# Kernel tuning notes

Measured on AMD Instinct MI355X. Metric: run time of the kernel, lower is better.

## Reference

```python
import jax, jax.numpy as jnp
import numpy as np

B_GRAPHS = 256
N_PER = 512
N = B_GRAPHS * N_PER            # 131072 nodes
E = 1048576                     # edges (avg degree 8)
H = 64                          # hidden_dim
L = 3                           # num_layers
R = 128                         # rnn_dim
NODE_IN = 2
EDGE_IN = 2
OUT = 2
JK = L * H


def setup_inputs() -> dict:
    key = jax.random.key(0)
    ks = jax.random.split(key, 40)
    # intra-graph random edges
    g = jax.random.randint(ks[0], (E,), 0, B_GRAPHS)
    src = g * N_PER + jax.random.randint(ks[1], (E,), 0, N_PER)
    dst = g * N_PER + jax.random.randint(ks[2], (E,), 0, N_PER)
    edge_index = jnp.stack([src, dst]).astype(jnp.int64)
    batch = jnp.repeat(jnp.arange(B_GRAPHS, dtype=jnp.int64), N_PER)

    p = lambda k, shp: jax.random.normal(k, shp, jnp.float32) * 0.1
    return dict(
        x=jax.random.normal(ks[3], (N, NODE_IN), jnp.float32),
        edge_attr=jax.random.normal(ks[4], (E, EDGE_IN), jnp.float32),
        node_W=p(ks[5], (NODE_IN, H)), node_b=p(ks[6], (H,)),
        edgeemb_W=p(ks[7], (EDGE_IN, H)), edgeemb_b=p(ks[8], (H,)),
        gat_W=p(ks[9], (L, H, H)), gat_Wedge=p(ks[10], (L, H, H)),
        gat_att_src=p(ks[11], (L, H)), gat_att_dst=p(ks[12], (L, H)),
        gat_att_edge=p(ks[13], (L, H)), gat_b=p(ks[14], (L, H)),
        gru_wih_f=p(ks[15], (3 * R, JK)), gru_whh_f=p(ks[16], (3 * R, R)),
        gru_bih_f=p(ks[17], (3 * R,)), gru_bhh_f=p(ks[18], (3 * R,)),
        gru_wih_b=p(ks[19], (3 * R, JK)), gru_whh_b=p(ks[20], (3 * R, R)),
        gru_bih_b=p(ks[21], (3 * R,)), gru_bhh_b=p(ks[22], (3 * R,)),
        head_W1=p(ks[23], (2 * R, 64)), head_b1=p(ks[24], (64,)),
        head_W2=p(ks[25], (64, OUT)), head_b2=p(ks[26], (OUT,)),
        edge_index=edge_index, batch=batch,
    )


def _gru_dir(xs, wih, whh, bih, bhh):
    # xs: [T, B, F] -> outputs [T, B, R]  (PyTorch GRU cell equations)
    gx = xs @ wih.T + bih  # precompute input gates [T, B, 3R]
    h0 = jnp.zeros((xs.shape[1], R), xs.dtype)

    def step(h, g):
        gh = h @ whh.T + bhh
        r = jax.nn.sigmoid(g[..., :R] + gh[..., :R])
        z = jax.nn.sigmoid(g[..., R:2 * R] + gh[..., R:2 * R])
        n = jnp.tanh(g[..., 2 * R:] + r * gh[..., 2 * R:])
        hn = (1.0 - z) * n + z * h
        return hn, hn

    _, ys = jax.lax.scan(step, h0, gx)
    return ys


def _forward(x, edge_attr, node_W, node_b, edgeemb_W, edgeemb_b,
             gat_W, gat_Wedge, gat_att_src, gat_att_dst, gat_att_edge, gat_b,
             gru_wih_f, gru_whh_f, gru_bih_f, gru_bhh_f,
             gru_wih_b, gru_whh_b, gru_bih_b, gru_bhh_b,
             head_W1, head_b1, head_W2, head_b2, edge_index, batch):
    src, dst = edge_index[0], edge_index[1]
    h = x @ node_W + node_b                     # [N, H]
    e = edge_attr @ edgeemb_W + edgeemb_b       # [E, H]

    # PyG GATConv default add_self_loops=True, fill_value='mean':
    # self-loop edge feature = mean of incoming edge features per node
    ones = jnp.ones((E,), e.dtype)
    deg = jax.ops.segment_sum(ones, dst, num_segments=N)
    e_loop = jax.ops.segment_sum(e, dst, num_segments=N) / jnp.maximum(deg, 1.0)[:, None]
    ar = jnp.arange(N, dtype=src.dtype)
    srcF = jnp.concatenate([src, ar])
    dstF = jnp.concatenate([dst, ar])
    eF = jnp.concatenate([e, e_loop], axis=0)   # [E+N, H]

    outs = []
    for l in range(L):
        xp = h @ gat_W[l]                                   # [N, H]
        a_s = xp @ gat_att_src[l]                           # [N]
        a_d = xp @ gat_att_dst[l]                           # [N]
        a_e = (eF @ gat_Wedge[l]) @ gat_att_edge[l]         # [E+N]
        alpha = jax.nn.leaky_relu(a_s[srcF] + a_d[dstF] + a_e, 0.2)
        m = jax.ops.segment_max(alpha, dstF, num_segments=N)
        ex = jnp.exp(alpha - m[dstF])
        den = jax.ops.segment_sum(ex, dstF, num_segments=N)
        w = ex / den[dstF]                                  # segment softmax
        agg = jax.ops.segment_sum(w[:, None] * xp[srcF], dstF, num_segments=N) + gat_b[l]
        h = jax.nn.leaky_relu(agg, 0.01)                    # F.leaky_relu default slope
        outs.append(h)

    h_jk = jnp.concatenate(outs, axis=-1)                   # [N, JK]
    # to_dense_batch: sorted equal-size graphs -> dense reshape, mask all True
    dense = h_jk.reshape(B_GRAPHS, N_PER, JK)
    xs = dense.transpose(1, 0, 2)                           # [T, B, JK]
    yf = _gru_dir(xs, gru_wih_f, gru_whh_f, gru_bih_f, gru_bhh_f)
    yb = _gru_dir(xs[::-1], gru_wih_b, gru_whh_b, gru_bih_b, gru_bhh_b)[::-1]
    rnn_out = jnp.concatenate([yf, yb], axis=-1).transpose(1, 0, 2)  # [B, T, 2R]
    out = jax.nn.relu(rnn_out @ head_W1 + head_b1) @ head_W2 + head_b2
    return out.reshape(N, OUT)                              # out[mask], mask full


def reference(x, edge_attr, node_W, node_b, edgeemb_W, edgeemb_b,
              gat_W, gat_Wedge, gat_att_src, gat_att_dst, gat_att_edge, gat_b,
              gru_wih_f, gru_whh_f, gru_bih_f, gru_bhh_f,
              gru_wih_b, gru_whh_b, gru_bih_b, gru_bhh_b,
              head_W1, head_b1, head_W2, head_b2, edge_index, batch):
    return _forward(x, edge_attr, node_W, node_b, edgeemb_W, edgeemb_b,
                    gat_W, gat_Wedge, gat_att_src, gat_att_dst, gat_att_edge, gat_b,
                    gru_wih_f, gru_whh_f, gru_bih_f, gru_bhh_f,
                    gru_wih_b, gru_whh_b, gru_bih_b, gru_bhh_b,
                    head_W1, head_b1, head_W2, head_b2, edge_index, batch)
```

## Files before the change

### kernel.cpp

```cpp
#include <hip/hip_runtime.h>
#include <cstdint>
#include <cstddef>

typedef _Float16 half_t;
typedef _Float16 half8 __attribute__((ext_vector_type(8)));
typedef float f32x4 __attribute__((ext_vector_type(4)));

constexpr int NN = 131072;
constexpr int NE = 1048576;
constexpr int NPER = 512;

#define DEVINL __device__ __forceinline__

DEVINL float sigm_(float x){ float e = __expf(-x); return __builtin_amdgcn_rcpf(1.f+e); }
DEVINL float tanh_(float x){
  x = fminf(15.f, fmaxf(-15.f, x));
  float e = __expf(-2.f*x);
  return (1.f-e)*__builtin_amdgcn_rcpf(1.f+e);
}

#define LDS_BARRIER() asm volatile("s_waitcnt lgkmcnt(0)\ns_barrier" ::: "memory")


__global__ void const_kernel(const float* __restrict__ gatWe,
                             const float* __restrict__ attE, const float* __restrict__ eW,
                             const float* __restrict__ eb, float* __restrict__ cc){
  int l = blockIdx.x, k = threadIdx.x;
  const float* Wel = gatWe + l*4096;
  float s3=0.f;
  for (int j=0;j<64;j++) s3 += Wel[k*64+j]*attE[l*64+j];
  float c0 = eW[k]*s3, c1 = eW[64+k]*s3, cb = eb[k]*s3;
  for (int off=1; off<64; off<<=1){
    c0 += __shfl_xor(c0,off); c1 += __shfl_xor(c1,off); cb += __shfl_xor(cb,off);
  }
  if (k==0){ cc[l]=c0; cc[3+l]=c1; cc[6+l]=cb; }
}

__global__ void prep_pack(const float* __restrict__ wih_f, const float* __restrict__ wih_b,
                          const float* __restrict__ head_W1, const float* __restrict__ gat_W,
                          const float* __restrict__ bih_f, const float* __restrict__ bih_b,
                          const float* __restrict__ whh_f, const float* __restrict__ whh_b,
                          half_t* __restrict__ BcombT, half_t* __restrict__ W1T,
                          half_t* __restrict__ BTgat, float* __restrict__ bias_comb,
                          half_t* __restrict__ whh16){
  int gid = blockIdx.x*256 + threadIdx.x;
  if (gid < 147456){
    int j = gid/192, k = gid%192;
    float v = (j<384)? wih_f[j*192+k] : wih_b[(j-384)*192+k];
    BcombT[gid] = (half_t)v;
  } else if (gid < 163840){
    int i = gid - 147456;
    int n = i>>8, k = i&255;
    W1T[i] = (half_t)head_W1[k*64+n];
  } else if (gid < 176128){
    int i = gid - 163840;
    int l = i>>12, r = i&4095;
    int n = r>>6, k = r&63;
    BTgat[i] = (half_t)gat_W[l*4096 + k*64 + n];
  } else if (gid < 176896){
    int i = gid - 176128;
    int j = (i<384)? i : i-384;
    bias_comb[i] = (i<384)? bih_f[j] : bih_b[j];
  } else if (gid < 275200){
    int i = gid - 176896;
    float v = (i<49152)? whh_f[i] : whh_b[i-49152];
    whh16[i] = (half_t)v;
  }
}

__global__ void bias_fold(const float* __restrict__ bhh_f, const float* __restrict__ bhh_b,
                          float* __restrict__ bias_comb){
  int i = threadIdx.x + blockIdx.x*256;
  if (i < 256)      bias_comb[i]       += bhh_f[i];
  else if (i < 512) bias_comb[i+128]   += bhh_b[i-256];
}

__global__ __launch_bounds__(256) void embed_kernel(const float* __restrict__ x,
                            const float* __restrict__ nW, const float* __restrict__ nb,
                            half_t* __restrict__ h){
  int gid = blockIdx.x*256 + threadIdx.x;
  int n = gid>>6, j = gid&63;
  float v = x[2*n]*nW[j] + x[2*n+1]*nW[64+j] + nb[j];
  h[(size_t)n*64+j] = (half_t)v;
}

__global__ __launch_bounds__(256) void deg_count(const int* __restrict__ ei,
                          int* __restrict__ deg, int* __restrict__ tmp){
  int e = blockIdx.x*256 + threadIdx.x;
  int dt = ei[NE+e];
  tmp[e] = atomicAdd(&deg[dt],1);
}

__global__ __launch_bounds__(256) void scan1(const int* __restrict__ deg, int* __restrict__ rowstart,
                      int* __restrict__ bsum){
  __shared__ int sc[256];
  int b=blockIdx.x, t=threadIdx.x, i=b*256+t;
  int v=deg[i]; sc[t]=v; __syncthreads();
  for (int off=1; off<256; off<<=1){
    int tv = (t>=off)? sc[t-off] : 0;
    __syncthreads(); sc[t]+=tv; __syncthreads();
  }
  rowstart[i]=sc[t]-v;
  if (t==255) bsum[b]=sc[255];
}
__global__ void scan2(int* __restrict__ bsum){
  __shared__ int sc[512];
  int t=threadIdx.x; int v=bsum[t]; sc[t]=v; __syncthreads();
  for (int off=1; off<512; off<<=1){
    int tv = (t>=off)? sc[t-off] : 0;
    __syncthreads(); sc[t]+=tv; __syncthreads();
  }
  bsum[t]=sc[t]-v;
}
__global__ __launch_bounds__(256) void scan3(int* __restrict__ rowstart, const int* __restrict__ bsum){
  int b=blockIdx.x, t=threadIdx.x, i=b*256+t;
  rowstart[i]+=bsum[b];
}

__global__ __launch_bounds__(256) void fill2(const int* __restrict__ ei, const float* __restrict__ ea,
                      const int* __restrict__ rowstart, const int* __restrict__ tmp,
                      int4* __restrict__ rec){
  int e = blockIdx.x*256 + threadIdx.x;
  int dt = ei[NE+e];
  int slot = rowstart[dt] + tmp[e];
  int4 r;
  r.x = ei[e];
  r.y = __float_as_int(ea[2*e]);
  r.z = __float_as_int(ea[2*e+1]);
  r.w = dt;
  rec[slot] = r;
}

__global__ __launch_bounds__(256) void means_kernel(const int* __restrict__ deg, const int* __restrict__ rowstart,
                         const int4* __restrict__ rec, float2* __restrict__ m01){
  int n = blockIdx.x*256 + threadIdx.x;
  int st = rowstart[n], cnt = deg[n];
  float s0=0.f, s1=0.f;
  for (int i=0;i<cnt;i++){
    int4 r = rec[st+i];
    s0 += __int_as_float(r.y);
    s1 += __int_as_float(r.z);
  }
  float inv = 1.f/(float)max(cnt,1);
  float2 m; m.x = s0*inv; m.y = s1*inv;
  m01[n] = m;
}

__global__ __launch_bounds__(256) void gemm_xp(const half_t* __restrict__ A, int lda,
                        const half_t* __restrict__ BT,
                        const float* __restrict__ attS, const float* __restrict__ attD,
                        half_t* __restrict__ xp, float* __restrict__ a_s, float* __restrict__ a_d){
  __shared__ half_t As[128*32];
  __shared__ half_t Bs[64*32];
  const int tid = threadIdx.x, m0 = blockIdx.x*128;
  const int w = tid>>6, lane = tid&63;
  const int lm = lane&15, quad = lane>>4;
  const int wm0 = w*32;
  f32x4 acc[2][4] = {};
  for (int k0=0;k0<64;k0+=32){
    {
      const int c0 = tid*2;
      #pragma unroll
      for (int u=0;u<2;u++){
        int c=c0+u; int row=c>>2; int off=(c&3)*8;
        *(half8*)(&As[row*32+off]) = *(const half8*)(&A[(size_t)(m0+row)*lda + k0 + off]);
      }
      int c=tid; int row=c>>2; int off=(c&3)*8;
      *(half8*)(&Bs[row*32+off]) = *(const half8*)(&BT[(size_t)row*64 + k0 + off]);
    }
    __syncthreads();
    half8 af[2], bf[4];
    #pragma unroll
    for (int nt=0;nt<4;nt++) bf[nt] = *(const half8*)(&Bs[(nt*16+lm)*32 + quad*8]);
    #pragma unroll
    for (int mt=0;mt<2;mt++) af[mt] = *(const half8*)(&As[(wm0+mt*16+lm)*32 + quad*8]);
    #pragma unroll
    for (int mt=0;mt<2;mt++)
      #pragma unroll
      for (int nt=0;nt<4;nt++)
        acc[mt][nt] = __builtin_amdgcn_mfma_f32_16x16x32_f16(af[mt], bf[nt], acc[mt][nt], 0,0,0);
    __syncthreads();
  }
  float vsv[4], vdv[4];
  #pragma unroll
  for (int nt=0;nt<4;nt++){ vsv[nt]=attS[nt*16+lm]; vdv[nt]=attD[nt*16+lm]; }
  #pragma unroll
  for (int mt=0;mt<2;mt++)
   #pragma unroll
   for (int r=0;r<4;r++){
    int m = m0+wm0+mt*16+quad*4+r;
    float ps=0.f, pd=0.f;
    #pragma unroll
    for (int nt=0;nt<4;nt++){
      float v = acc[mt][nt][r];
      xp[(size_t)m*64 + nt*16+lm] = (half_t)v;
      ps += v*vsv[nt]; pd += v*vdv[nt];
    }
    ps += __shfl_xor(ps,1); ps += __shfl_xor(ps,2); ps += __shfl_xor(ps,4); ps += __shfl_xor(ps,8);
    pd += __shfl_xor(pd,1); pd += __shfl_xor(pd,2); pd += __shfl_xor(pd,4); pd += __shfl_xor(pd,8);
    if (lm==0){ a_s[m]=ps; a_d[m]=pd; }
  }
}

__global__ __launch_bounds__(256) void edge_w(const int4* __restrict__ rec,
                       const float* __restrict__ a_s, const float* __restrict__ a_d,
                       const float* __restrict__ cc, int l, int2* __restrict__ sw,
                       const int* __restrict__ deg, const float2* __restrict__ m01,
                       float* __restrict__ wsf){
  int b = blockIdx.x;
  if (b < 4096){
    int s = b*256 + threadIdx.x;
    int4 r = rec[s];
    float al = a_s[r.x] + a_d[r.w]
             + __int_as_float(r.y)*cc[l] + __int_as_float(r.z)*cc[3+l] + cc[6+l];
    al = al>0.f? al : 0.2f*al;
    int2 o;
    o.x = (r.x & 511) | ((r.w & 127) << 16);
    o.y = __float_as_int(__expf(al));
    sw[s] = o;
  } else {
    int n = (b-4096)*256 + threadIdx.x;
    int cnt = deg[n];
    float2 m = m01[n];
    float ael = cnt? (m.x*cc[l] + m.y*cc[3+l] + cc[6+l]) : 0.f;
    float asl = a_s[n] + a_d[n] + ael;
    asl = asl>0.f? asl : 0.2f*asl;
    wsf[n] = __expf(asl);
  }
}

constexpr int SWCAP = 1536;
__global__ __launch_bounds__(512,4) void agg_lds(const int* __restrict__ rowstart, const int* __restrict__ deg,
                          const int2* __restrict__ sw, const float* __restrict__ wsf, int l,
                          const half_t* __restrict__ xp, const float* __restrict__ bias,
                          half_t* __restrict__ hjk){
  __shared__ int2  swl[SWCAP];
  __shared__ float nwsf[128];
  __shared__ int   ncnt[128];
  const int tid = threadIdx.x;
  const int nbase = blockIdx.x*128;
  const half_t* __restrict__ xpg = xp + ((size_t)(nbase >> 9))*32768;
  const int segst = rowstart[nbase];
  const int segend = rowstart[nbase+127] + deg[nbase+127];
  const int segcnt = segend - segst;
  const int w = tid>>6, lane = tid&63;
  int scap = segcnt < SWCAP ? segcnt : SWCAP;
  for (int i=tid; i<scap; i+=512) swl[i] = sw[segst+i];
  if (tid < 128){
    nwsf[tid] = wsf[nbase + tid];
    ncnt[tid] = deg[nbase + tid];
  }
  const int e0 = rowstart[nbase + w*16] - segst;
  const int e1 = (w==7) ? segcnt : (rowstart[nbase + w*16 + 16] - segst);
  __syncthreads();
  const float bv = bias[lane];
  const int nlb = nbase & 511;

  auto flush = [&](int cur, float acc, float den){
    float wv = nwsf[cur];
    float xs = (float)xpg[(size_t)(nlb + cur)*64 + lane];
    float v = (acc + wv*xs)/(den + wv) + bv;
    v = v>0.f? v : 0.01f*v;
    hjk[(size_t)(nbase + cur)*192 + l*64 + lane] = (half_t)v;
  };

  if (segcnt <= SWCAP){
    if (e0 < e1){
      int2 p = swl[e0];
      float xv = (float)xpg[(size_t)(p.x & 511)*64 + lane];
      int cur = p.x >> 16;
      float acc = 0.f, den = 0.f;
      for (int e = e0; e < e1; ++e){
        int en = (e+1 < e1) ? e+1 : e;
        int2 pn = swl[en];
        float xvn = (float)xpg[(size_t)(pn.x & 511)*64 + lane];
        int dl = p.x >> 16;
        if (dl != cur){
          flush(cur, acc, den);
          cur = dl; acc = 0.f; den = 0.f;
        }
        float ww = __int_as_float(p.y);
        acc += ww*xv; den += ww;
        p = pn; xv = xvn;
      }
      flush(cur, acc, den);
    }
    #pragma unroll
    for (int i=0;i<16;i++){
      int li = w*16+i;
      if (ncnt[li]==0) flush(li, 0.f, 0.f);
    }
  } else {
    if (e0 < e1){
      int2 p = sw[segst+e0];
      float xv = (float)xpg[(size_t)(p.x & 511)*64 + lane];
      int cur = p.x >> 16;
      float acc = 0.f, den = 0.f;
      for (int e = e0; e < e1; ++e){
        int en = (e+1 < e1) ? e+1 : e;
        int2 pn = sw[segst+en];
        float xvn = (float)xpg[(size_t)(pn.x & 511)*64 + lane];
        int dl = p.x >> 16;
        if (dl != cur){
          flush(cur, acc, den);
          cur = dl; acc = 0.f; den = 0.f;
        }
        float ww = __int_as_float(p.y);
        acc += ww*xv; den += ww;
        p = pn; xv = xvn;
      }
      flush(cur, acc, den);
    }
    #pragma unroll
    for (int i=0;i<16;i++){
      int li = w*16+i;
      if (ncnt[li]==0) flush(li, 0.f, 0.f);
    }
  }
}

__global__ __launch_bounds__(256) void gemm_head(const half_t* __restrict__ A,
                        const half_t* __restrict__ W1T, const float* __restrict__ b1,
                        const float* __restrict__ W2, const float* __restrict__ b2,
                        float* __restrict__ out){
  __shared__ half_t As[128*32];
  __shared__ half_t Bs[64*32];
  const int tid = threadIdx.x, m0 = blockIdx.x*128;
  const int w = tid>>6, lane = tid&63;
  const int lm = lane&15, quad = lane>>4;
  const int wm0 = w*32;
  f32x4 acc[2][4] = {};
  for (int k0=0;k0<256;k0+=32){
    {
      const int c0 = tid*2;
      #pragma unroll
      for (int u=0;u<2;u++){
        int c=c0+u; int row=c>>2; int off=(c&3)*8;
        *(half8*)(&As[row*32+off]) = *(const half8*)(&A[(size_t)(m0+row)*256 + k0 + off]);
      }
      int c=tid; int row=c>>2; int off=(c&3)*8;
      *(half8*)(&Bs[row*32+off]) = *(const half8*)(&W1T[(size_t)row*256 + k0 + off]);
    }
    __syncthreads();
    half8 af[2], bf[4];
    #pragma unroll
    for (int nt=0;nt<4;nt++) bf[nt] = *(const half8*)(&Bs[(nt*16+lm)*32 + quad*8]);
    #pragma unroll
    for (int mt=0;mt<2;mt++) af[mt] = *(const half8*)(&As[(wm0+mt*16+lm)*32 + quad*8]);
    #pragma unroll
    for (int mt=0;mt<2;mt++)
      #pragma unroll
      for (int nt=0;nt<4;nt++)
        acc[mt][nt] = __builtin_amdgcn_mfma_f32_16x16x32_f16(af[mt], bf[nt], acc[mt][nt], 0,0,0);
    __syncthreads();
  }
  float b1v[4], w20[4], w21[4];
  #pragma unroll
  for (int nt=0;nt<4;nt++){
    int n = nt*16+lm;
    b1v[nt]=b1[n]; w20[nt]=W2[n*2]; w21[nt]=W2[n*2+1];
  }
  float b20=b2[0], b21=b2[1];
  #pragma unroll
  for (int mt=0;mt<2;mt++)
   #pragma unroll
   for (int r=0;r<4;r++){
    int m = m0+wm0+mt*16+quad*4+r;
    float p0=0.f, p1=0.f;
    #pragma unroll
    for (int nt=0;nt<4;nt++){
      float v = acc[mt][nt][r] + b1v[nt];
      v = v>0.f? v : 0.f;
      p0 += v*w20[nt]; p1 += v*w21[nt];
    }
    p0 += __shfl_xor(p0,1); p0 += __shfl_xor(p0,2); p0 += __shfl_xor(p0,4); p0 += __shfl_xor(p0,8);
    p1 += __shfl_xor(p1,1); p1 += __shfl_xor(p1,2); p1 += __shfl_xor(p1,4); p1 += __shfl_xor(p1,8);
    if (lm==0){
      out[(size_t)m*2]   = p0 + b20;
      out[(size_t)m*2+1] = p1 + b21;
    }
  }
}

__global__ __launch_bounds__(512,1) void gru_fused(
    const half_t* __restrict__ whh16, const float* __restrict__ bhh_f, const float* __restrict__ bhh_b,
    const half_t* __restrict__ gxf, const half_t* __restrict__ gxb,
    float* __restrict__ hstate, half_t* __restrict__ y, int c, int gruBlocks,
    const half_t* __restrict__ hjk, const half_t* __restrict__ BcombT, const float* __restrict__ biasc,
    half_t* __restrict__ gxf_n, half_t* __restrict__ gxb_n, int s0f, int s0b){
  __shared__ __align__(16) char SMEM[16384];
  const int bid = blockIdx.x;
  const int tid = threadIdx.x;
  if (bid < gruBlocks){
    __builtin_amdgcn_s_setprio(1);
    auto& H = *(half_t (*)[2][16][132])SMEM;
    half_t* slab0 = (half_t*)(SMEM + 8448);
    half_t* slab1 = (half_t*)(SMEM + 8448 + 3072);

    const int d = bid >> 6, gblk = bid & 63;
    const half_t* __restrict__ gx = d ? gxb : gxf;
    const float* bhh = d ? bhh_b : bhh_f;
    const int w = tid >> 6, lane = tid & 63;
    const int l15 = lane & 15, quad = lane >> 4;
    const int unit = w*16 + l15;

    half8 bf[3][4];
    float bhn = bhh[256 + unit];
    {
      const half_t* wbase = whh16 + (size_t)d*49152;
      #pragma unroll
      for (int g=0; g<3; g++){
        const half_t* wp = wbase + (size_t)(g*128 + unit)*128;
        #pragma unroll
        for (int kk=0; kk<4; kk++)
          bf[g][kk] = *(const half8*)(wp + kk*32 + quad*8);
      }
    }

    float hreg = hstate[((size_t)d*256 + gblk*4 + quad)*128 + unit];

    const bool loader = (w >= 4 && w < 7);
    const int jsl = d ? -384 : 384;
    int idx8 = 0;
    const half_t* srcp = nullptr;
    if (loader){
      int idx = (w-4)*64 + lane;
      int g_loc = idx/48, o = idx - g_loc*48;
      idx8 = idx*8;
      int j0 = d ? 127 : 0;
      srcp = gx + ((size_t)(gblk*4 + g_loc)*128 + j0)*384 + o*8;
    }

    const int cgg = tid >> 6;
    const int cpart = (tid & 63)*2;
    const int pos0 = d ? (511 - c*128) : (c*128);
    const int ystep = d ? -256 : 256;
    half_t* yptr = y + ((size_t)(gblk*4 + cgg)*512 + pos0)*256 + d*128 + cpart;

    for (int i=tid; i<2112; i+=512) ((uint*)SMEM)[i] = 0;
    LDS_BARRIER();
    H[0][quad*4][unit] = (half_t)hreg;
    half8 lvA, lvB;
    if (loader){
      lvA = *(const half8*)srcp; srcp += jsl;
      *(half8*)(slab0 + idx8) = lvA;
      lvB = *(const half8*)srcp; srcp += jsl;
    }
    LDS_BARRIER();

    auto stepf = [&](const half_t* cs, half_t* ns, int rd, int wr2,
                     half8& lvI, half8& lvW, bool pfi, bool pfw, bool cp){
      if (loader && pfi){ lvI = *(const half8*)srcp; srcp += jsl; }
      if (cp && tid < 256){
        uint hv = *(const uint*)&H[rd][cgg*4][cpart];
        *(uint*)yptr = hv;
        yptr += ystep;
      }
      float g0 = (float)cs[quad*384 + unit];
      float g1 = (float)cs[quad*384 + 128 + unit];
      float g2 = (float)cs[quad*384 + 256 + unit];
      half8 af[4] = {};
      if ((l15 & 3) == 0){
        #pragma unroll
        for (int kk=0; kk<4; kk++)
          af[kk] = *(const half8*)&H[rd][l15][kk*32 + quad*8];
      }
      f32x4 P[3] = {};
      #pragma unroll
      for (int kk=0; kk<4; kk++)
        #pragma unroll
        for (int g=0; g<3; g++)
          P[g] = __builtin_amdgcn_mfma_f32_16x16x32_f16(af[kk], bf[g][kk], P[g], 0,0,0);
      float rr = sigm_(g0 + P[0][0]);
      float zz = sigm_(g1 + P[1][0]);
      float nn = tanh_(g2 + rr*(P[2][0] + bhn));
      float hn = nn + zz*(hreg - nn);
      hreg = hn;
      H[wr2][quad*4][unit] = (half_t)hn;
      if (loader && pfw) *(half8*)(ns + idx8) = lvW;
      LDS_BARRIER();
    };

    stepf(slab0, slab1, 0,1, lvA, lvB, true,  true,  false);
    stepf(slab1, slab0, 1,0, lvB, lvA, true,  true,  true);
    for (int it=1; it<63; it++){
      stepf(slab0, slab1, 0,1, lvA, lvB, true, true, true);
      stepf(slab1, slab0, 1,0, lvB, lvA, true, true, true);
    }
    stepf(slab0, slab1, 0,1, lvA, lvB, false, true,  true);
    stepf(slab1, slab0, 1,0, lvB, lvA, false, false, true);
    if (tid < 256){
      uint hv = *(const uint*)&H[0][cgg*4][cpart];
      *(uint*)yptr = hv;
    }
    __builtin_amdgcn_s_setprio(0);
    hstate[((size_t)d*256 + gblk*4 + quad)*128 + unit] = hreg;
  } else {
    half_t* As = (half_t*)SMEM;
    half_t* Bs = (half_t*)(SMEM + 8192);
    const int gb = bid - gruBlocks;
    const int bx = gb & 255, by = gb >> 8;
    const int m0 = bx*128;
    const bool back = by >= 3;
    const int n0 = (back ? by-3 : by)*128;
    const int step0 = back ? s0b : s0f;
    half_t* C = back ? gxb_n : gxf_n;
    const half_t* BTh = BcombT + (back ? (size_t)384*192 : 0);
    const float* bh = biasc + (back ? 384 : 0);
    const int w = tid>>6, lane = tid&63;
    const int lm = lane&15, quad = lane>>4;
    const int wm0 = (w>>2)*64, wn0 = (w&3)*32;
    f32x4 acc[4][2] = {};
    for (int k0=0; k0<192; k0+=32){
      {
        int cidx = tid; int row = cidx>>2; int off = (cidx&3)*8;
        int m = m0+row;
        size_t arow = (size_t)(m>>7)*512 + step0 + (m&127);
        *(half8*)(&As[row*32+off]) = *(const half8*)(&hjk[arow*192 + k0 + off]);
        *(half8*)(&Bs[row*32+off]) = *(const half8*)(&BTh[(size_t)(n0+row)*192 + k0 + off]);
      }
      __syncthreads();
      half8 af[4], bfr[2];
      #pragma unroll
      for (int nt=0;nt<2;nt++) bfr[nt] = *(const half8*)(&Bs[(wn0+nt*16+lm)*32 + quad*8]);
      #pragma unroll
      for (int mt=0;mt<4;mt++) af[mt] = *(const half8*)(&As[(wm0+mt*16+lm)*32 + quad*8]);
      #pragma unroll
      for (int mt=0;mt<4;mt++)
        #pragma unroll
        for (int nt=0;nt<2;nt++)
          acc[mt][nt] = __builtin_amdgcn_mfma_f32_16x16x32_f16(af[mt], bfr[nt], acc[mt][nt], 0,0,0);
      __syncthreads();
    }
    #pragma unroll
    for (int mt=0;mt<4;mt++)
     #pragma unroll
     for (int nt=0;nt<2;nt++)
      #pragma unroll
      for (int r=0;r<4;r++){
        int m = m0+wm0+mt*16+quad*4+r;
        int n = n0+wn0+nt*16+lm;
        float v = acc[mt][nt][r] + bh[n];
        C[(size_t)m*384 + n] = (half_t)v;
      }
  }
}

extern "C" void kernel_launch(void* const* d_in, const int* in_sizes, int n_in,
                              void* d_out, int out_size, void* d_ws, size_t ws_size,
                              hipStream_t stream) {
  const float* x       = (const float*)d_in[0];
  const float* ea      = (const float*)d_in[1];
  const float* node_W  = (const float*)d_in[2];
  const float* node_b  = (const float*)d_in[3];
  const float* eW      = (const float*)d_in[4];
  const float* eb      = (const float*)d_in[5];
  const float* gat_W   = (const float*)d_in[6];
  const float* gat_We  = (const float*)d_in[7];
  const float* attS    = (const float*)d_in[8];
  const float* attD    = (const float*)d_in[9];
  const float* attE    = (const float*)d_in[10];
  const float* gat_b   = (const float*)d_in[11];
  const float* wih_f   = (const float*)d_in[12];
  const float* whh_f   = (const float*)d_in[13];
  const float* bih_f   = (const float*)d_in[14];
  const float* bhh_f   = (const float*)d_in[15];
  const float* wih_b   = (const float*)d_in[16];
  const float* whh_b   = (const float*)d_in[17];
  const float* bih_b   = (const float*)d_in[18];
  const float* bhh_b   = (const float*)d_in[19];
  const float* head_W1 = (const float*)d_in[20];
  const float* head_b1 = (const float*)d_in[21];
  const float* head_W2 = (const float*)d_in[22];
  const float* head_b2 = (const float*)d_in[23];
  const int*   ei      = (const int*)d_in[24];
  float* out = (float*)d_out;
  char* ws = (char*)d_ws;
  (void)in_sizes; (void)n_in; (void)out_size; (void)ws_size;

  size_t o = 0;
  auto alloc = [&](size_t bytes)->size_t{ size_t r=o; o += (bytes+255)&~(size_t)255; return r; };
  size_t o_cc     = alloc(16*4);
  size_t o_biasc  = alloc(768*4);
  size_t o_BcombT = alloc((size_t)768*192*2);
  size_t o_BTgat  = alloc((size_t)3*4096*2);
  size_t o_W1T    = alloc((size_t)64*256*2);
  size_t o_whh16  = alloc((size_t)2*49152*2);
  size_t o_hstate = alloc((size_t)2*256*128*4);
  size_t shared_base = o;

  size_t o_deg    = alloc((size_t)NN*4);
  size_t zero_end = o;
  size_t o_tmp    = alloc((size_t)NE*4);
  size_t o_rows   = alloc((size_t)NN*4);
  size_t o_bsum   = alloc(512*4);
  size_t o_rec    = alloc((size_t)NE*16);
  size_t o_sw     = alloc((size_t)NE*8);
  size_t o_m01    = alloc((size_t)NN*8);
  size_t o_as     = alloc((size_t)NN*4);
  size_t o_ad     = alloc((size_t)NN*4);
  size_t o_wsf    = alloc((size_t)NN*4);
  size_t o_h      = alloc((size_t)NN*64*2);
  size_t o_xp     = alloc((size_t)NN*64*2);
  size_t gat_end  = o;
  size_t gat_size = gat_end - shared_base;

  const size_t GXC    = (size_t)256*128*384*2;
  const size_t HJK_SZ = (size_t)NN*192*2;
  size_t shared_sz = gat_size > 4*GXC ? gat_size : 4*GXC;
  size_t o_gx0f = shared_base;
  size_t o_gx0b = shared_base + GXC;
  size_t o_gx1f = shared_base + 2*GXC;
  size_t o_gx1b = shared_base + 3*GXC;
  size_t o_hjk = shared_base + shared_sz;
  size_t o_y   = o_hjk + HJK_SZ;

  int*    deg    = (int*)(ws+o_deg);
  int*    tmp    = (int*)(ws+o_tmp);
  int*    rows   = (int*)(ws+o_rows);
  int*    bsum   = (int*)(ws+o_bsum);
  int4*   rec    = (int4*)(ws+o_rec);
  int2*   sw     = (int2*)(ws+o_sw);
  float2* m01    = (float2*)(ws+o_m01);
  float*  a_s    = (float*)(ws+o_as);
  float*  a_d    = (float*)(ws+o_ad);
  float*  wsf    = (float*)(ws+o_wsf);
  float*  cc     = (float*)(ws+o_cc);
  float*  biasc  = (float*)(ws+o_biasc);
  half_t* h      = (half_t*)(ws+o_h);
  half_t* xp     = (half_t*)(ws+o_xp);
  half_t* hjk    = (half_t*)(ws+o_hjk);
  half_t* BcombT = (half_t*)(ws+o_BcombT);
  half_t* BTgat  = (half_t*)(ws+o_BTgat);
  half_t* W1T    = (half_t*)(ws+o_W1T);
  half_t* whh16  = (half_t*)(ws+o_whh16);
  float*  hstate = (float*)(ws+o_hstate);
  half_t* gxbuf[2][2] = {{(half_t*)(ws+o_gx0f), (half_t*)(ws+o_gx0b)},
                         {(half_t*)(ws+o_gx1f), (half_t*)(ws+o_gx1b)}};
  half_t* y      = (half_t*)(ws+o_y);

  hipMemsetAsync(ws+shared_base, 0, zero_end-shared_base, stream);
  hipMemsetAsync(ws+o_hstate, 0, (size_t)2*256*128*4, stream);

  const_kernel<<<3,64,0,stream>>>(gat_We, attE, eW, eb, cc);
  prep_pack<<<1075,256,0,stream>>>(wih_f, wih_b, head_W1, gat_W, bih_f, bih_b, whh_f, whh_b,
                                   BcombT, W1T, BTgat, biasc, whh16);
  bias_fold<<<2,256,0,stream>>>(bhh_f, bhh_b, biasc);
  embed_kernel<<<32768,256,0,stream>>>(x, node_W, node_b, h);
  deg_count<<<4096,256,0,stream>>>(ei, deg, tmp);
  scan1<<<512,256,0,stream>>>(deg, rows, bsum);
  scan2<<<1,512,0,stream>>>(bsum);
  scan3<<<512,256,0,stream>>>(rows, bsum);
  fill2<<<4096,256,0,stream>>>(ei, ea, rows, tmp, rec);
  means_kernel<<<512,256,0,stream>>>(deg, rows, rec, m01);

  for (int l=0;l<3;l++){
    const half_t* in = (l==0)? h : (hjk + (size_t)(l-1)*64);
    int lda = (l==0)? 64 : 192;
    gemm_xp<<<1024,256,0,stream>>>(in, lda, BTgat + (size_t)l*4096, attS + l*64, attD + l*64, xp, a_s, a_d);
    edge_w<<<4608,256,0,stream>>>(rec, a_s, a_d, cc, l, sw, deg, m01, wsf);
    agg_lds<<<1024,512,0,stream>>>(rows, deg, sw, wsf, l, xp, gat_b + l*64, hjk);
  }

  gru_fused<<<1536,512,0,stream>>>(whh16, bhh_f, bhh_b, gxbuf[0][0], gxbuf[0][1], hstate, y, 0, 0,
                                   hjk, BcombT, biasc, gxbuf[0][0], gxbuf[0][1], 0, 384);
  for (int c=0;c<4;c++){
    int buf = c&1, nbuf = (c+1)&1;
    int grid = 128 + (c<3 ? 1536 : 0);
    gru_fused<<<grid,512,0,stream>>>(whh16, bhh_f, bhh_b, gxbuf[buf][0], gxbuf[buf][1], hstate, y, c, 128,
                                     hjk, BcombT, biasc, gxbuf[nbuf][0], gxbuf[nbuf][1],
                                     (c+1)*128, (2-c)*128);
  }

  gemm_head<<<1024,256,0,stream>>>(y, W1T, head_b1, head_W2, head_b2, out);
}
```

Baseline: 784.4 us.

## Deepen edge-gather prefetch and load GRU gates directly into registers

The small-segment GAT aggregation loop now keeps an 8-deep register prefetch ring of edge records and gathered features instead of a single lookahead, so more gathers are in flight at once. In the GRU recurrence, the LDS slab staging of precomputed input gates by loader waves is removed. Each thread instead loads its own three gate values straight from global memory two steps ahead. The MFMA chain is also split into two independent accumulator chains to shorten the dependency latency per step. This trades more registers and more scattered scalar global loads for fewer LDS writes and reads, and it drops the LDS zero-fill.

```diff
diff --git a/kernel.cpp b/kernel.cpp
--- a/kernel.cpp
+++ b/kernel.cpp
@@ -265,23 +265,41 @@
   };
 
   if (segcnt <= SWCAP){
-    if (e0 < e1){
-      int2 p = swl[e0];
-      float xv = (float)xpg[(size_t)(p.x & 511)*64 + lane];
-      int cur = p.x >> 16;
+    const int cnt = e1 - e0;
+    if (cnt > 0){
+      int2  P[8];
+      float X[8];
+      #pragma unroll
+      for (int i=0;i<8;i++){
+        int idx = e0 + (i < cnt ? i : cnt-1);
+        P[i] = swl[idx];
+        X[i] = (float)xpg[(size_t)(P[i].x & 511)*64 + lane];
+      }
+      int cur = P[0].x >> 16;
       float acc = 0.f, den = 0.f;
-      for (int e = e0; e < e1; ++e){
-        int en = (e+1 < e1) ? e+1 : e;
-        int2 pn = swl[en];
-        float xvn = (float)xpg[(size_t)(pn.x & 511)*64 + lane];
-        int dl = p.x >> 16;
-        if (dl != cur){
-          flush(cur, acc, den);
-          cur = dl; acc = 0.f; den = 0.f;
+      int e = e0;
+      for (; e + 8 <= e1; e += 8){
+        #pragma unroll
+        for (int i=0;i<8;i++){
+          int dl = P[i].x >> 16;
+          if (dl != cur){ flush(cur, acc, den); cur = dl; acc = 0.f; den = 0.f; }
+          float ww = __int_as_float(P[i].y);
+          acc += ww*X[i]; den += ww;
+          int nidx = e + 8 + i;
+          int cidx = nidx < e1 ? nidx : e1-1;
+          P[i] = swl[cidx];
+          X[i] = (float)xpg[(size_t)(P[i].x & 511)*64 + lane];
         }
-        float ww = __int_as_float(p.y);
-        acc += ww*xv; den += ww;
-        p = pn; xv = xvn;
+      }
+      int rem = e1 - e;
+      #pragma unroll
+      for (int i=0;i<8;i++){
+        if (i < rem){
+          int dl = P[i].x >> 16;
+          if (dl != cur){ flush(cur, acc, den); cur = dl; acc = 0.f; den = 0.f; }
+          float ww = __int_as_float(P[i].y);
+          acc += ww*X[i]; den += ww;
+        }
       }
       flush(cur, acc, den);
     }
@@ -394,8 +412,6 @@
   if (bid < gruBlocks){
     __builtin_amdgcn_s_setprio(1);
     auto& H = *(half_t (*)[2][16][132])SMEM;
-    half_t* slab0 = (half_t*)(SMEM + 8448);
-    half_t* slab1 = (half_t*)(SMEM + 8448 + 3072);
 
     const int d = bid >> 6, gblk = bid & 63;
     const half_t* __restrict__ gx = d ? gxb : gxf;
@@ -419,76 +435,68 @@
 
     float hreg = hstate[((size_t)d*256 + gblk*4 + quad)*128 + unit];
 
-    const bool loader = (w >= 4 && w < 7);
-    const int jsl = d ? -384 : 384;
-    int idx8 = 0;
-    const half_t* srcp = nullptr;
-    if (loader){
-      int idx = (w-4)*64 + lane;
-      int g_loc = idx/48, o = idx - g_loc*48;
-      idx8 = idx*8;
-      int j0 = d ? 127 : 0;
-      srcp = gx + ((size_t)(gblk*4 + g_loc)*128 + j0)*384 + o*8;
-    }
+    const int jstep = d ? -384 : 384;
+    const int ystep = d ? -256 : 256;
+    const int j0 = d ? 127 : 0;
+    const int pos0 = d ? (511 - c*128) : (c*128);
 
     const int cgg = tid >> 6;
     const int cpart = (tid & 63)*2;
-    const int pos0 = d ? (511 - c*128) : (c*128);
-    const int ystep = d ? -256 : 256;
     half_t* yptr = y + ((size_t)(gblk*4 + cgg)*512 + pos0)*256 + d*128 + cpart;
 
-    for (int i=tid; i<2112; i+=512) ((uint*)SMEM)[i] = 0;
+    long gofs = ((long)(gblk*4 + quad)*128 + j0)*384 + unit;
+    half_t gA0,gA1,gA2, gB0,gB1,gB2;
+    gA0 = gx[gofs]; gA1 = gx[gofs+128]; gA2 = gx[gofs+256]; gofs += jstep;
+    gB0 = gx[gofs]; gB1 = gx[gofs+128]; gB2 = gx[gofs+256]; gofs += jstep;
+
+    H[0][quad*4][unit] = (half_t)hreg;
     LDS_BARRIER();
-    H[0][quad*4][unit] = (half_t)hreg;
-    half8 lvA, lvB;
-    if (loader){
-      lvA = *(const half8*)srcp; srcp += jsl;
-      *(half8*)(slab0 + idx8) = lvA;
-      lvB = *(const half8*)srcp; srcp += jsl;
-    }
-    LDS_BARRIER();
-
-    auto stepf = [&](const half_t* cs, half_t* ns, int rd, int wr2,
-                     half8& lvI, half8& lvW, bool pfi, bool pfw, bool cp){
-      if (loader && pfi){ lvI = *(const half8*)srcp; srcp += jsl; }
+
+    auto stepf = [&](int rd, int wr2, half_t& c0, half_t& c1, half_t& c2,
+                     bool cp, bool pf){
       if (cp && tid < 256){
         uint hv = *(const uint*)&H[rd][cgg*4][cpart];
         *(uint*)yptr = hv;
         yptr += ystep;
       }
-      float g0 = (float)cs[quad*384 + unit];
-      float g1 = (float)cs[quad*384 + 128 + unit];
-      float g2 = (float)cs[quad*384 + 256 + unit];
       half8 af[4] = {};
       if ((l15 & 3) == 0){
         #pragma unroll
         for (int kk=0; kk<4; kk++)
           af[kk] = *(const half8*)&H[rd][l15][kk*32 + quad*8];
       }
-      f32x4 P[3] = {};
-      #pragma unroll
-      for (int kk=0; kk<4; kk++)
-        #pragma unroll
-        for (int g=0; g<3; g++)
-          P[g] = __builtin_amdgcn_mfma_f32_16x16x32_f16(af[kk], bf[g][kk], P[g], 0,0,0);
-      float rr = sigm_(g0 + P[0][0]);
-      float zz = sigm_(g1 + P[1][0]);
-      float nn = tanh_(g2 + rr*(P[2][0] + bhn));
+      f32x4 Pa[3] = {}, Pb[3] = {};
+      #pragma unroll
+      for (int g=0; g<3; g++){
+        Pa[g] = __builtin_amdgcn_mfma_f32_16x16x32_f16(af[0], bf[g][0], Pa[g], 0,0,0);
+        Pb[g] = __builtin_amdgcn_mfma_f32_16x16x32_f16(af[2], bf[g][2], Pb[g], 0,0,0);
+        Pa[g] = __builtin_amdgcn_mfma_f32_16x16x32_f16(af[1], bf[g][1], Pa[g], 0,0,0);
+        Pb[g] = __builtin_amdgcn_mfma_f32_16x16x32_f16(af[3], bf[g][3], Pb[g], 0,0,0);
+      }
+      float p0 = Pa[0][0] + Pb[0][0];
+      float p1 = Pa[1][0] + Pb[1][0];
+      float p2 = Pa[2][0] + Pb[2][0];
+      float rr = sigm_((float)c0 + p0);
+      float zz = sigm_((float)c1 + p1);
+      float nn = tanh_((float)c2 + rr*(p2 + bhn));
       float hn = nn + zz*(hreg - nn);
       hreg = hn;
       H[wr2][quad*4][unit] = (half_t)hn;
-      if (loader && pfw) *(half8*)(ns + idx8) = lvW;
+      if (pf){
+        c0 = gx[gofs]; c1 = gx[gofs+128]; c2 = gx[gofs+256];
+        gofs += jstep;
+      }
       LDS_BARRIER();
     };
 
-    stepf(slab0, slab1, 0,1, lvA, lvB, true,  true,  false);
-    stepf(slab1, slab0, 1,0, lvB, lvA, true,  true,  true);
+    stepf(0,1, gA0,gA1,gA2, false, true);
+    stepf(1,0, gB0,gB1,gB2, true,  true);
     for (int it=1; it<63; it++){
-      stepf(slab0, slab1, 0,1, lvA, lvB, true, true, true);
-      stepf(slab1, slab0, 1,0, lvB, lvA, true, true, true);
-    }
-    stepf(slab0, slab1, 0,1, lvA, lvB, false, true,  true);
-    stepf(slab1, slab0, 1,0, lvB, lvA, false, false, true);
+      stepf(0,1, gA0,gA1,gA2, true, true);
+      stepf(1,0, gB0,gB1,gB2, true, true);
+    }
+    stepf(0,1, gA0,gA1,gA2, true, false);
+    stepf(1,0, gB0,gB1,gB2, true, false);
     if (tid < 256){
       uint hv = *(const uint*)&H[0][cgg*4][cpart];
       *(uint*)yptr = hv;
```

New measurement: 709.3 us. 1.11x faster.
